# Performance work log

Measured on AMD Instinct MI355X. Metric: run time of the kernel, lower is better.

Reference implementation:

```python
import jax, jax.numpy as jnp
import numpy as np

N_NODES = 50000
N_EDGES = 800000
NODE_DIM = 256
EDGE_DIM = 64
HIDDEN = 512
OUT_DIM = 256


def setup_inputs() -> dict:
    key = jax.random.key(0)
    ks = jax.random.split(key, 6)
    node_features = jax.random.normal(ks[0], (N_NODES, NODE_DIM), dtype=jnp.float32)
    edge_index = jax.random.randint(ks[1], (2, N_EDGES), 0, N_NODES, dtype=jnp.int64)
    edge_features = jax.random.normal(ks[2], (N_EDGES, EDGE_DIM), dtype=jnp.float32)
    in_dim = EDGE_DIM + NODE_DIM
    W1 = jax.random.normal(ks[3], (in_dim, HIDDEN), dtype=jnp.float32) * (1.0 / np.sqrt(in_dim))
    b1 = jnp.zeros((HIDDEN,), dtype=jnp.float32)
    W2 = jax.random.normal(ks[4], (HIDDEN, OUT_DIM), dtype=jnp.float32) * (1.0 / np.sqrt(HIDDEN))
    b2 = jnp.zeros((OUT_DIM,), dtype=jnp.float32)
    return {"node_features": node_features, "edge_index": edge_index,
            "edge_features": edge_features, "W1": W1, "b1": b1, "W2": W2, "b2": b2}


def reference(node_features, edge_index, edge_features, W1, b1, W2, b2):
    # edge_direction='in' -> scatter edge features to target nodes (row 1)
    tgt = edge_index[1]
    # mean aggregation: segment-sum of features and counts, clamp counts at 1
    agg = jax.ops.segment_sum(edge_features, tgt, num_segments=N_NODES)  # [N, E_dim]
    counts = jax.ops.segment_sum(jnp.ones((edge_features.shape[0],), edge_features.dtype),
                                 tgt, num_segments=N_NODES)
    agg = agg / jnp.maximum(counts, 1.0)[:, None]
    combined = jnp.concatenate([agg, node_features], axis=1)  # [N, edge+node]
    h = jax.nn.relu(combined @ W1 + b1)  # dropout=0 -> identity
    out = h @ W2 + b2  # [N, OUT_DIM]
    return out
```

## Files before the change

kernel.cpp:

```cpp
#include <hip/hip_runtime.h>
#include <hip/hip_bf16.h>

#define N_NODES 50000
#define N_EDGES 800000
#define NODE_DIM 256
#define EDGE_DIM 64
#define HIDDEN 512
#define OUT_DIM 256
#define IN_DIM 320

typedef __bf16 bf16_t;
typedef bf16_t bf16x8 __attribute__((ext_vector_type(8)));
typedef float floatx4 __attribute__((ext_vector_type(4)));

__device__ inline bf16_t to_bf16(float f) {
    __hip_bfloat16 h = __float2bfloat16(f);
    bf16_t b;
    __builtin_memcpy(&b, &h, 2);
    return b;
}

__global__ __launch_bounds__(256) void scatter_edges(
    const float* __restrict__ ef, const int* __restrict__ eidx,
    float* __restrict__ agg, float* __restrict__ counts) {
    int gid = blockIdx.x * 256 + threadIdx.x;
    int e = gid >> 6;
    int d = gid & 63;
    if (e >= N_EDGES) return;
    int t = eidx[N_EDGES + e];
    t = min(max(t, 0), N_NODES - 1);
    float v = ef[(size_t)e * EDGE_DIM + d];
    atomicAdd(&agg[(size_t)t * EDGE_DIM + d], v);
    if (d == 0) atomicAdd(&counts[t], 1.0f);
}

__global__ __launch_bounds__(256) void build_combined(
    const float* __restrict__ agg, const float* __restrict__ counts,
    const float* __restrict__ node, bf16_t* __restrict__ combined) {
    int idx = blockIdx.x * 256 + threadIdx.x;
    if (idx >= N_NODES * IN_DIM) return;
    int i = idx / IN_DIM;
    int d = idx - i * IN_DIM;
    float v;
    if (d < EDGE_DIM) {
        float c = counts[i];
        v = agg[(size_t)i * EDGE_DIM + d] / fmaxf(c, 1.0f);
    } else {
        v = node[(size_t)i * NODE_DIM + (d - EDGE_DIM)];
    }
    combined[idx] = to_bf16(v);
}

__global__ __launch_bounds__(256) void convert_weights(
    const float* __restrict__ W1, const float* __restrict__ W2,
    bf16_t* __restrict__ W1T, bf16_t* __restrict__ W2T) {
    int idx = blockIdx.x * 256 + threadIdx.x;
    if (idx < IN_DIM * HIDDEN) {
        int k = idx / HIDDEN, n = idx - k * HIDDEN;
        W1T[(size_t)n * IN_DIM + k] = to_bf16(W1[idx]);
    } else {
        int j = idx - IN_DIM * HIDDEN;
        if (j < HIDDEN * OUT_DIM) {
            int k = j / OUT_DIM, n = j - k * OUT_DIM;
            W2T[(size_t)n * HIDDEN + k] = to_bf16(W2[j]);
        }
    }
}

template <bool RELU, bool OUT_BF16>
__global__ __launch_bounds__(256) void gemm_bt(
    const bf16_t* __restrict__ A, const bf16_t* __restrict__ BT,
    const float* __restrict__ bias, void* __restrict__ Cout,
    int M, int N, int K) {
    __shared__ bf16_t As[128][40];
    __shared__ bf16_t Bs[128][40];

    const int tid = threadIdx.x;
    const int lane = tid & 63;
    const int w = tid >> 6;
    const int wm = (w & 1) * 64;
    const int wn = (w >> 1) * 64;
    const int lrow = lane & 15;
    const int quad = lane >> 4;
    const int kq = quad * 8;
    const int m0 = blockIdx.x * 128;
    const int n0 = blockIdx.y * 128;

    floatx4 acc[4][4] = {};

    const int nkt = K / 32;
    for (int kt = 0; kt < nkt; ++kt) {
        const int k0 = kt * 32;
        __syncthreads();
#pragma unroll
        for (int it = 0; it < 2; ++it) {
            int slot = tid + it * 256;
            int row = slot >> 2;
            int cg = (slot & 3) * 8;
            int gm = m0 + row;
            uint4 va = {0u, 0u, 0u, 0u};
            if (gm < M)
                va = *reinterpret_cast<const uint4*>(&A[(size_t)gm * K + k0 + cg]);
            *reinterpret_cast<uint4*>(&As[row][cg]) = va;
            int gn = n0 + row;
            uint4 vb = *reinterpret_cast<const uint4*>(&BT[(size_t)gn * K + k0 + cg]);
            *reinterpret_cast<uint4*>(&Bs[row][cg]) = vb;
        }
        __syncthreads();

        bf16x8 af[4], bfr[4];
#pragma unroll
        for (int mi = 0; mi < 4; ++mi)
            af[mi] = *reinterpret_cast<const bf16x8*>(&As[wm + mi * 16 + lrow][kq]);
#pragma unroll
        for (int ni = 0; ni < 4; ++ni)
            bfr[ni] = *reinterpret_cast<const bf16x8*>(&Bs[wn + ni * 16 + lrow][kq]);
#pragma unroll
        for (int mi = 0; mi < 4; ++mi)
#pragma unroll
            for (int ni = 0; ni < 4; ++ni)
                acc[mi][ni] = __builtin_amdgcn_mfma_f32_16x16x32_bf16(
                    af[mi], bfr[ni], acc[mi][ni], 0, 0, 0);
    }

#pragma unroll
    for (int ni = 0; ni < 4; ++ni) {
        int gn = n0 + wn + ni * 16 + lrow;
        float bv = bias[gn];
#pragma unroll
        for (int mi = 0; mi < 4; ++mi) {
            int gmb = m0 + wm + mi * 16 + quad * 4;
#pragma unroll
            for (int r = 0; r < 4; ++r) {
                int gm = gmb + r;
                if (gm < M) {
                    float v = acc[mi][ni][r] + bv;
                    if (RELU) v = fmaxf(v, 0.0f);
                    if (OUT_BF16)
                        ((bf16_t*)Cout)[(size_t)gm * N + gn] = to_bf16(v);
                    else
                        ((float*)Cout)[(size_t)gm * N + gn] = v;
                }
            }
        }
    }
}

extern "C" void kernel_launch(void* const* d_in, const int* in_sizes, int n_in,
                              void* d_out, int out_size, void* d_ws, size_t ws_size,
                              hipStream_t stream) {
    const float* node = (const float*)d_in[0];
    const int* eidx = (const int*)d_in[1];
    const float* ef = (const float*)d_in[2];
    const float* W1 = (const float*)d_in[3];
    const float* b1 = (const float*)d_in[4];
    const float* W2 = (const float*)d_in[5];
    const float* b2 = (const float*)d_in[6];
    float* out = (float*)d_out;

    char* ws = (char*)d_ws;
    float* agg = (float*)ws;
    float* counts = (float*)(ws + 12800000);
    bf16_t* combined = (bf16_t*)(ws + 13000000);
    bf16_t* h = (bf16_t*)(ws + 45000000);
    bf16_t* W1T = (bf16_t*)(ws + 96200000);
    bf16_t* W2T = (bf16_t*)(ws + 96527680);

    hipMemsetAsync(ws, 0, 13000000, stream);

    scatter_edges<<<(N_EDGES * 64) / 256, 256, 0, stream>>>(ef, eidx, agg, counts);

    build_combined<<<(N_NODES * IN_DIM + 255) / 256, 256, 0, stream>>>(
        agg, counts, node, combined);

    convert_weights<<<(IN_DIM * HIDDEN + HIDDEN * OUT_DIM + 255) / 256, 256, 0, stream>>>(
        W1, W2, W1T, W2T);

    gemm_bt<true, true><<<dim3((N_NODES + 127) / 128, HIDDEN / 128), 256, 0, stream>>>(
        combined, W1T, b1, (void*)h, N_NODES, HIDDEN, IN_DIM);

    gemm_bt<false, false><<<dim3((N_NODES + 127) / 128, OUT_DIM / 128), 256, 0, stream>>>(
        h, W2T, b2, (void*)out, N_NODES, OUT_DIM, HIDDEN);
}
```

Measured before the change: 609.5 us.

## Replace atomic edge scatter with CSR sort-and-gather; use async LDS loads in GEMM

The per-element float atomic scatter of edge features is replaced by a counting sort: a count histogram, a single-block scan into offsets, an edge-id scatter, and a per-node wave gather. The gather sums its edges, divides by the count and writes the bf16 combined row directly, so the separate build_combined pass goes away. This removes 51M float atomics and the agg buffer round trip, at the cost of more kernel launches and random 256-byte gathers. Separately, the GEMM tile loads now use global_load_lds async copies into unpadded shared tiles, which may bring back LDS bank conflicts on the fragment reads.

```diff
diff --git a/kernel.cpp b/kernel.cpp
--- a/kernel.cpp
+++ b/kernel.cpp
@@ -20,35 +20,89 @@
     return b;
 }
 
-__global__ __launch_bounds__(256) void scatter_edges(
-    const float* __restrict__ ef, const int* __restrict__ eidx,
-    float* __restrict__ agg, float* __restrict__ counts) {
-    int gid = blockIdx.x * 256 + threadIdx.x;
-    int e = gid >> 6;
-    int d = gid & 63;
+__device__ inline void async16(const void* g, void* l) {
+    __builtin_amdgcn_global_load_lds(
+        (const __attribute__((address_space(1))) unsigned int*)g,
+        (__attribute__((address_space(3))) unsigned int*)l, 16, 0, 0);
+}
+
+__global__ __launch_bounds__(256) void hist_counts(
+    const int* __restrict__ eidx, int* __restrict__ counts) {
+    int e = blockIdx.x * 256 + threadIdx.x;
     if (e >= N_EDGES) return;
-    int t = eidx[N_EDGES + e];
-    t = min(max(t, 0), N_NODES - 1);
-    float v = ef[(size_t)e * EDGE_DIM + d];
-    atomicAdd(&agg[(size_t)t * EDGE_DIM + d], v);
-    if (d == 0) atomicAdd(&counts[t], 1.0f);
-}
-
-__global__ __launch_bounds__(256) void build_combined(
-    const float* __restrict__ agg, const float* __restrict__ counts,
-    const float* __restrict__ node, bf16_t* __restrict__ combined) {
-    int idx = blockIdx.x * 256 + threadIdx.x;
-    if (idx >= N_NODES * IN_DIM) return;
-    int i = idx / IN_DIM;
-    int d = idx - i * IN_DIM;
-    float v;
-    if (d < EDGE_DIM) {
-        float c = counts[i];
-        v = agg[(size_t)i * EDGE_DIM + d] / fmaxf(c, 1.0f);
-    } else {
-        v = node[(size_t)i * NODE_DIM + (d - EDGE_DIM)];
-    }
-    combined[idx] = to_bf16(v);
+    int t = min(max(eidx[N_EDGES + e], 0), N_NODES - 1);
+    atomicAdd(&counts[t], 1);
+}
+
+__global__ __launch_bounds__(256) void scan_offsets(
+    const int* __restrict__ counts, int* __restrict__ offsets,
+    int* __restrict__ cursor) {
+    __shared__ int sums[256];
+    const int t = threadIdx.x;
+    const int CH = (N_NODES + 255) / 256;
+    const int base = t * CH;
+    int s = 0;
+    for (int i = 0; i < CH; ++i) {
+        int idx = base + i;
+        if (idx < N_NODES) s += counts[idx];
+    }
+    sums[t] = s;
+    __syncthreads();
+    for (int off = 1; off < 256; off <<= 1) {
+        int v = (t >= off) ? sums[t - off] : 0;
+        __syncthreads();
+        sums[t] += v;
+        __syncthreads();
+    }
+    int run = (t == 0) ? 0 : sums[t - 1];
+    for (int i = 0; i < CH; ++i) {
+        int idx = base + i;
+        if (idx < N_NODES) {
+            offsets[idx] = run;
+            cursor[idx] = run;
+            run += counts[idx];
+        }
+    }
+    if (t == 255) offsets[N_NODES] = sums[255];
+}
+
+__global__ __launch_bounds__(256) void scatter_ids(
+    const int* __restrict__ eidx, int* __restrict__ cursor,
+    int* __restrict__ sorted) {
+    int e = blockIdx.x * 256 + threadIdx.x;
+    if (e >= N_EDGES) return;
+    int t = min(max(eidx[N_EDGES + e], 0), N_NODES - 1);
+    int pos = atomicAdd(&cursor[t], 1);
+    sorted[pos] = e;
+}
+
+__global__ __launch_bounds__(256) void gather_combined(
+    const float* __restrict__ ef, const int* __restrict__ sorted,
+    const int* __restrict__ offsets, const float* __restrict__ node,
+    bf16_t* __restrict__ combined) {
+    int wave = (blockIdx.x * 256 + threadIdx.x) >> 6;
+    int lane = threadIdx.x & 63;
+    if (wave >= N_NODES) return;
+    int beg = offsets[wave], end = offsets[wave + 1];
+    float acc = 0.f;
+    int j = beg;
+    for (; j + 1 < end; j += 2) {
+        int e0 = sorted[j], e1 = sorted[j + 1];
+        float v0 = ef[(size_t)e0 * EDGE_DIM + lane];
+        float v1 = ef[(size_t)e1 * EDGE_DIM + lane];
+        acc += v0 + v1;
+    }
+    if (j < end) {
+        int e0 = sorted[j];
+        acc += ef[(size_t)e0 * EDGE_DIM + lane];
+    }
+    float inv = 1.0f / (float)max(end - beg, 1);
+    size_t cb = (size_t)wave * IN_DIM;
+    combined[cb + lane] = to_bf16(acc * inv);
+    const float* nf = node + (size_t)wave * NODE_DIM;
+#pragma unroll
+    for (int c = 0; c < 4; ++c)
+        combined[cb + EDGE_DIM + c * 64 + lane] = to_bf16(nf[c * 64 + lane]);
 }
 
 __global__ __launch_bounds__(256) void convert_weights(
@@ -72,8 +126,8 @@
     const bf16_t* __restrict__ A, const bf16_t* __restrict__ BT,
     const float* __restrict__ bias, void* __restrict__ Cout,
     int M, int N, int K) {
-    __shared__ bf16_t As[128][40];
-    __shared__ bf16_t Bs[128][40];
+    __shared__ bf16_t As[128][32];
+    __shared__ bf16_t Bs[128][32];
 
     const int tid = threadIdx.x;
     const int lane = tid & 63;
@@ -94,17 +148,12 @@
         __syncthreads();
 #pragma unroll
         for (int it = 0; it < 2; ++it) {
-            int slot = tid + it * 256;
+            int slot = it * 256 + tid;
             int row = slot >> 2;
             int cg = (slot & 3) * 8;
-            int gm = m0 + row;
-            uint4 va = {0u, 0u, 0u, 0u};
-            if (gm < M)
-                va = *reinterpret_cast<const uint4*>(&A[(size_t)gm * K + k0 + cg]);
-            *reinterpret_cast<uint4*>(&As[row][cg]) = va;
-            int gn = n0 + row;
-            uint4 vb = *reinterpret_cast<const uint4*>(&BT[(size_t)gn * K + k0 + cg]);
-            *reinterpret_cast<uint4*>(&Bs[row][cg]) = vb;
+            int gm = min(m0 + row, M - 1);
+            async16(&A[(size_t)gm * K + k0 + cg], (bf16_t*)As + slot * 8);
+            async16(&BT[(size_t)(n0 + row) * K + k0 + cg], (bf16_t*)Bs + slot * 8);
         }
         __syncthreads();
 
@@ -159,19 +208,22 @@
     float* out = (float*)d_out;
 
     char* ws = (char*)d_ws;
-    float* agg = (float*)ws;
-    float* counts = (float*)(ws + 12800000);
-    bf16_t* combined = (bf16_t*)(ws + 13000000);
-    bf16_t* h = (bf16_t*)(ws + 45000000);
-    bf16_t* W1T = (bf16_t*)(ws + 96200000);
-    bf16_t* W2T = (bf16_t*)(ws + 96527680);
-
-    hipMemsetAsync(ws, 0, 13000000, stream);
-
-    scatter_edges<<<(N_EDGES * 64) / 256, 256, 0, stream>>>(ef, eidx, agg, counts);
-
-    build_combined<<<(N_NODES * IN_DIM + 255) / 256, 256, 0, stream>>>(
-        agg, counts, node, combined);
+    int* counts = (int*)ws;
+    int* offsets = (int*)(ws + 200000);
+    int* cursor = (int*)(ws + 400016);
+    int* sorted = (int*)(ws + 600016);
+    bf16_t* combined = (bf16_t*)(ws + 3800032);
+    bf16_t* h = (bf16_t*)(ws + 35800032);
+    bf16_t* W1T = (bf16_t*)(ws + 87000032);
+    bf16_t* W2T = (bf16_t*)(ws + 87327712);
+
+    hipMemsetAsync(counts, 0, 200000, stream);
+
+    hist_counts<<<(N_EDGES + 255) / 256, 256, 0, stream>>>(eidx, counts);
+    scan_offsets<<<1, 256, 0, stream>>>(counts, offsets, cursor);
+    scatter_ids<<<(N_EDGES + 255) / 256, 256, 0, stream>>>(eidx, cursor, sorted);
+    gather_combined<<<(N_NODES * 64 + 255) / 256, 256, 0, stream>>>(
+        ef, sorted, offsets, node, combined);
 
     convert_weights<<<(IN_DIM * HIDDEN + HIDDEN * OUT_DIM + 255) / 256, 256, 0, stream>>>(
         W1, W2, W1T, W2T);
```

Measured after the change: 712.0 us. 1.17x slower.
